# Optimization experiments

Hardware: AMD Instinct MI355X
Metric: run time of the kernel (lower is better)

Reference implementation:

```python
import jax, jax.numpy as jnp
import numpy as np

D_HEAD = 64
KV_HEADS = 8
Q_HEADS = 32
ROPE_BASE = 10000.0


def rope(x):
    # x: (B, S, H, D); pairs are interleaved along last dim, matching torch view(...,D//2,2)
    B, S, H, D = x.shape
    inv_freq = 1.0 / (ROPE_BASE ** (jnp.arange(0, D, 2, dtype=jnp.float32) / D))
    theta = jnp.arange(S, dtype=jnp.float32)[:, None] * inv_freq[None, :]  # (S, D/2)
    cos = jnp.cos(theta)[None, :, None, :]
    sin = jnp.sin(theta)[None, :, None, :]
    xf = x.astype(jnp.float32).reshape(B, S, H, D // 2, 2)
    x1, x2 = xf[..., 0], xf[..., 1]
    out = jnp.stack((x1 * cos - x2 * sin, x1 * sin + x2 * cos), axis=-1)
    return out.reshape(B, S, H, D).astype(x.dtype)


def setup_inputs() -> dict:
    key = jax.random.key(0)
    ks = jax.random.split(key, 5)
    B, S, D = 2, 2048, 2048
    scale = 1.0 / np.sqrt(D)
    return {
        "x": jax.random.normal(ks[0], (B, S, D), dtype=jnp.float32),
        "Wq": jax.random.normal(ks[1], (Q_HEADS * D_HEAD, D), dtype=jnp.float32) * scale,
        "Wk": jax.random.normal(ks[2], (KV_HEADS * D_HEAD, D), dtype=jnp.float32) * scale,
        "Wv": jax.random.normal(ks[3], (KV_HEADS * D_HEAD, D), dtype=jnp.float32) * scale,
        "Wo": jax.random.normal(ks[4], (D, D), dtype=jnp.float32) * scale,
    }


def reference(x, Wq, Wk, Wv, Wo):
    B, S, D = x.shape
    G = Q_HEADS // KV_HEADS  # query heads per kv head

    Q = (x @ Wq.T).reshape(B, S, Q_HEADS, D_HEAD)
    K = (x @ Wk.T).reshape(B, S, KV_HEADS, D_HEAD)
    V = (x @ Wv.T).reshape(B, S, KV_HEADS, D_HEAD)

    Q = rope(Q)
    K = rope(K)

    # (B, KV, G, S, Dh): group g of kv head h corresponds to q head h*G+g,
    # exactly matching repeat_interleave of K/V along head dim.
    Q = Q.transpose(0, 2, 1, 3).reshape(B, KV_HEADS, G, S, D_HEAD)
    K = K.transpose(0, 2, 1, 3)  # (B, KV, S, Dh)
    V = V.transpose(0, 2, 1, 3)

    scores = jnp.einsum("bkgsd,bktd->bkgst", Q, K) / np.sqrt(D_HEAD).astype(np.float32)
    causal_mask = jnp.tril(jnp.ones((S, S), dtype=bool))
    scores = jnp.where(causal_mask, scores, -jnp.inf)
    probs = jax.nn.softmax(scores, axis=-1)
    attn = jnp.einsum("bkgst,bktd->bkgsd", probs, V)

    attn = attn.reshape(B, Q_HEADS, S, D_HEAD).transpose(0, 2, 1, 3).reshape(B, S, D)
    return attn @ Wo.T
```

## Files before the change

kernel.cpp:

```cpp
#include <hip/hip_runtime.h>
#include <stdint.h>

#define S_LEN   2048
#define D_MODEL 2048
#define DKV     512

typedef __attribute__((ext_vector_type(8))) short short8;
typedef __attribute__((ext_vector_type(4))) float f32x4;

__device__ static inline unsigned short f2bf(float f) {
  unsigned u = __builtin_bit_cast(unsigned, f);
  u += 0x7FFFu + ((u >> 16) & 1u);
  return (unsigned short)(u >> 16);
}
__device__ static inline float bf2f(unsigned short h) {
  return __builtin_bit_cast(float, ((unsigned)h) << 16);
}
__device__ static inline unsigned packtrunc2(float f0, float f1) {
  return __builtin_amdgcn_perm(__builtin_bit_cast(unsigned, f1),
                               __builtin_bit_cast(unsigned, f0), 0x07060302u);
}

__device__ static inline void gload_lds16(const void* g, void* lds) {
  __builtin_amdgcn_global_load_lds((const __attribute__((address_space(1))) void*)g,
                                   (__attribute__((address_space(3))) void*)lds,
                                   16, 0, 0);
}

template <int N>
__device__ __forceinline__ void wait_vm() {
  if constexpr (N == 8)      asm volatile("s_waitcnt vmcnt(8)" ::: "memory");
  else if constexpr (N == 6) asm volatile("s_waitcnt vmcnt(6)" ::: "memory");
  else if constexpr (N == 4) asm volatile("s_waitcnt vmcnt(4)" ::: "memory");
  else if constexpr (N == 3) asm volatile("s_waitcnt vmcnt(3)" ::: "memory");
  else                       asm volatile("s_waitcnt vmcnt(0)" ::: "memory");
}

__global__ __launch_bounds__(256) void cvt_all_kernel(
    const float* __restrict__ x, const float* __restrict__ wq, const float* __restrict__ wk,
    const float* __restrict__ wv, const float* __restrict__ wo,
    unsigned short* __restrict__ xb, unsigned short* __restrict__ wqb,
    unsigned short* __restrict__ wkb, unsigned short* __restrict__ wvb,
    unsigned short* __restrict__ wob) {
  int i = blockIdx.x * 256 + threadIdx.x;
  const float* s; unsigned short* d;
  if (i < 1048576)      { s = x;  d = xb;  }
  else if (i < 1572864) { s = wq; d = wqb; i -= 1048576; }
  else if (i < 1703936) { s = wk; d = wkb; i -= 1572864; }
  else if (i < 1835008) { s = wv; d = wvb; i -= 1703936; }
  else                  { s = wo; d = wob; i -= 1835008; }
  const float4 a = ((const float4*)s)[i * 2];
  const float4 b = ((const float4*)s)[i * 2 + 1];
  unsigned short u[8] = {f2bf(a.x), f2bf(a.y), f2bf(a.z), f2bf(a.w),
                         f2bf(b.x), f2bf(b.y), f2bf(b.z), f2bf(b.w)};
  *(uint4*)(d + (size_t)i * 8) = *(const uint4*)u;
}

template <int BM, int CMODE, typename CT>
__device__ __forceinline__ void gemm_deep_body(
    const unsigned short* __restrict__ A, int lda,
    const unsigned short* __restrict__ B, int ldb,
    CT* __restrict__ C, int ldc, int m0, int n0, unsigned short* ldsu) {
  constexpr int MI = BM / 32;
  constexpr int NI = 4;
  constexpr int A_BYTES = BM * 64;
  constexpr int B_BYTES = 256 * 64;
  constexpr int TILE_BYTES = A_BYTES + B_BYTES;
  constexpr int AL = BM / 128;
  constexpr int LOADS = AL + 2;
  constexpr int VMS = 2 * LOADS;

  const int tid  = threadIdx.x;
  const int lane = tid & 63;
  const int w    = tid >> 6;
  const int wm   = w >> 2;
  const int wn   = w & 3;
  const int lcol = lane & 15;
  const int lq   = lane >> 4;
  char* const ldsb = (char*)ldsu;

  const int sl   = (lane & 7) ^ (lane >> 3);
  const int colg = (sl & 3) * 8;
  const unsigned short* gA[AL];
  const unsigned short* gB[2];
#pragma unroll
  for (int L = 0; L < AL; ++L) {
    const int r = 2 * (L * 64 + w * 8 + (lane >> 3)) + (sl >> 2);
    gA[L] = A + (size_t)(m0 + r) * lda + colg;
  }
#pragma unroll
  for (int L = 0; L < 2; ++L) {
    const int r = 2 * (L * 64 + w * 8 + (lane >> 3)) + (sl >> 2);
    gB[L] = B + (size_t)(n0 + r) * ldb + colg;
  }

  auto stage = [&](int tt) {
    char* const sb = ldsb + (tt & 3) * TILE_BYTES;
#pragma unroll
    for (int L = 0; L < AL; ++L)
      gload_lds16(gA[L] + tt * 32, sb + L * 8192 + w * 1024);
#pragma unroll
    for (int L = 0; L < 2; ++L)
      gload_lds16(gB[L] + tt * 32, sb + A_BYTES + L * 8192 + w * 1024);
  };

  const int sR    = (((lcol & 1) << 2) | lq) ^ ((lcol >> 1) & 7);
  const int rdoff = (lcol >> 1) * 128 + sR * 16;

  f32x4 acc[MI][NI] = {};

  auto compute_tile = [&](char* buf) {
    short8 af[MI], bfr[NI];
#pragma unroll
    for (int mi = 0; mi < MI; ++mi)
      af[mi] = *(const short8*)(buf + wm * (MI * 1024) + mi * 1024 + rdoff);
#pragma unroll
    for (int ni = 0; ni < NI; ++ni)
      bfr[ni] = *(const short8*)(buf + A_BYTES + wn * 4096 + ni * 1024 + rdoff);
    __builtin_amdgcn_s_setprio(1);
#pragma unroll
    for (int mi = 0; mi < MI; ++mi)
#pragma unroll
      for (int ni = 0; ni < NI; ++ni)
        acc[mi][ni] = __builtin_amdgcn_mfma_f32_16x16x32_bf16(af[mi], bfr[ni], acc[mi][ni], 0, 0, 0);
    __builtin_amdgcn_s_setprio(0);
  };

  stage(0); stage(1); stage(2);

#define GPHASE(T, VMW, DOSTG)                          \
  do {                                                 \
    wait_vm<VMW>();                                    \
    __builtin_amdgcn_s_barrier();                      \
    asm volatile("" ::: "memory");                     \
    __builtin_amdgcn_sched_barrier(0);                 \
    if (DOSTG) stage((T) + 3);                         \
    compute_tile(ldsb + ((T) & 3) * TILE_BYTES);       \
  } while (0)

  for (int t4 = 0; t4 < 15; ++t4) {
    const int t = t4 * 4;
    GPHASE(t + 0, VMS, true);
    GPHASE(t + 1, VMS, true);
    GPHASE(t + 2, VMS, true);
    GPHASE(t + 3, VMS, true);
  }
  GPHASE(60, VMS,   true);
  GPHASE(61, VMS,   false);
  GPHASE(62, LOADS, false);
  GPHASE(63, 0,     false);
#undef GPHASE

#pragma unroll
  for (int mi = 0; mi < MI; ++mi)
#pragma unroll
    for (int ni = 0; ni < NI; ++ni)
#pragma unroll
      for (int r = 0; r < 4; ++r) {
        const int row = m0 + wm * (MI * 16) + mi * 16 + lq * 4 + r;
        const int col = n0 + wn * 64 + ni * 16 + lcol;
        if constexpr (CMODE == 1) {
          C[((size_t)((row >> 11) * 512 + col)) * 2048 + (row & 2047)] = f2bf(acc[mi][ni][r]);
        } else if constexpr (CMODE == 2) {
          C[(size_t)row * ldc + col] = acc[mi][ni][r];
        } else {
          C[(size_t)row * ldc + col] = f2bf(acc[mi][ni][r]);
        }
      }
}

__global__ __launch_bounds__(512, 2) void qkv_gemm_kernel(
    const unsigned short* __restrict__ x,
    const unsigned short* __restrict__ Wq, const unsigned short* __restrict__ Wk,
    const unsigned short* __restrict__ Wv,
    unsigned short* __restrict__ Qo, unsigned short* __restrict__ Ko,
    unsigned short* __restrict__ Vt) {
  extern __shared__ __align__(16) unsigned short lds[];
  const int bid = blockIdx.x;
  const int swz = (bid & 7) * 24 + (bid >> 3);
  const int mt = swz / 12, nt = swz % 12;
  const int m0 = mt * 256;
  if (nt < 8)
    gemm_deep_body<256, 0, unsigned short>(x, D_MODEL, Wq, D_MODEL, Qo, D_MODEL, m0, nt * 256, lds);
  else if (nt < 10)
    gemm_deep_body<256, 0, unsigned short>(x, D_MODEL, Wk, D_MODEL, Ko, DKV, m0, (nt - 8) * 256, lds);
  else
    gemm_deep_body<256, 1, unsigned short>(x, D_MODEL, Wv, D_MODEL, Vt, DKV, m0, (nt - 10) * 256, lds);
}

__global__ __launch_bounds__(512, 2) void oproj_gemm_kernel(
    const unsigned short* __restrict__ A, const unsigned short* __restrict__ Wo,
    float* __restrict__ C) {
  extern __shared__ __align__(16) unsigned short lds[];
  const int bid = blockIdx.x;
  const int swz = (bid & 7) * 32 + (bid >> 3);
  const int mt = swz >> 3, nt = swz & 7;
  gemm_deep_body<128, 2, float>(A, D_MODEL, Wo, D_MODEL, C, D_MODEL, mt * 128, nt * 256, lds);
}

__global__ __launch_bounds__(256) void rope_both_kernel(unsigned short* __restrict__ Qb,
                                                        unsigned short* __restrict__ Kb) {
  int idx = blockIdx.x * 256 + threadIdx.x;
  unsigned short* X; int lgHalf; float scale;
  if (idx < 4194304) { X = Qb; lgHalf = 10; scale = 0.1803368801111244f; }
  else               { X = Kb; lgHalf = 8;  scale = 1.0f; idx -= 4194304; }
  const int half = 1 << lgHalf;
  const int r  = idx >> lgHalf;
  const int cp = idx & (half - 1);
  const int i  = cp & 31;
  const int s  = r & (S_LEN - 1);
  const float inv = exp2f(-13.287712379549449f * (float)(2 * i) * (1.0f / 64.0f));
  const float th  = (float)s * inv;
  const float c = cosf(th), sn = sinf(th);
  unsigned short* p = X + ((size_t)r << (lgHalf + 1)) + 2 * cp;
  const float x0 = bf2f(p[0]), x1 = bf2f(p[1]);
  p[0] = f2bf((x0 * c - x1 * sn) * scale);
  p[1] = f2bf((x0 * sn + x1 * c) * scale);
}

__global__ __launch_bounds__(256, 2) void attn_kernel(const unsigned short* __restrict__ Q,
                                                      const unsigned short* __restrict__ K,
                                                      const unsigned short* __restrict__ Vt,
                                                      unsigned short* __restrict__ O) {
  const int hq = blockIdx.y;
  const int bb = blockIdx.z;
  const int hk = hq >> 2;
  const int tid  = threadIdx.x;
  const int lane = tid & 63;
  const int w    = tid >> 6;
  const int lcol = lane & 15;
  const int lq   = lane >> 4;
  const int trow = tid >> 2;
  const int tq   = (tid & 3) * 16;

  const int X = blockIdx.x;
  const int qt[4] = {X, 15 - X, 16 + X, 31 - X};

  __shared__ unsigned short Ks[64 * 72];
  __shared__ unsigned short Vts[64 * 72];
  __shared__ unsigned short Ps[4][64 * 72];

  const int prow = w * 16 + lcol;

  uint4 kp0, kp1, vp0, vp1;
  {
    const unsigned short* gk = K + ((size_t)(bb * S_LEN + trow)) * DKV + hk * 64 + tq;
    kp0 = *(const uint4*)gk; kp1 = *(const uint4*)(gk + 8);
    const unsigned short* gv = Vt + ((size_t)(bb * DKV + hk * 64 + trow)) * S_LEN + tq;
    vp0 = *(const uint4*)gv; vp1 = *(const uint4*)(gv + 8);
  }

#pragma unroll
  for (int j = 0; j < 4; ++j) {
    const unsigned short* g = Q + ((size_t)(bb * S_LEN + qt[j] * 64 + trow)) * D_MODEL + hq * 64 + tq;
    *(uint4*)&Ps[j][trow * 72 + tq]     = *(const uint4*)g;
    *(uint4*)&Ps[j][trow * 72 + tq + 8] = *(const uint4*)(g + 8);
  }
  asm volatile("s_waitcnt lgkmcnt(0)" ::: "memory");

  short8 qf[4][2];
#pragma unroll
  for (int j = 0; j < 4; ++j)
#pragma unroll
    for (int ks = 0; ks < 2; ++ks)
      qf[j][ks] = *(const short8*)&Ps[j][prow * 72 + ks * 32 + lq * 8];

  f32x4 Oacc[4][4] = {};
  float lacc[4] = {0.f, 0.f, 0.f, 0.f};

  const int tmax = qt[3];
  for (int t = 0; t <= tmax; ++t) {
    __syncthreads();
    *(uint4*)&Ks[trow * 72 + tq]      = kp0;
    *(uint4*)&Ks[trow * 72 + tq + 8]  = kp1;
    *(uint4*)&Vts[trow * 72 + tq]     = vp0;
    *(uint4*)&Vts[trow * 72 + tq + 8] = vp1;
    if (t < tmax) {
      const int t1 = (t + 1) * 64;
      const unsigned short* gk = K + ((size_t)(bb * S_LEN + t1 + trow)) * DKV + hk * 64 + tq;
      kp0 = *(const uint4*)gk; kp1 = *(const uint4*)(gk + 8);
      const unsigned short* gv = Vt + ((size_t)(bb * DKV + hk * 64 + trow)) * S_LEN + t1 + tq;
      vp0 = *(const uint4*)gv; vp1 = *(const uint4*)(gv + 8);
    }
    __syncthreads();

    bool act[4];
#pragma unroll
    for (int j = 0; j < 4; ++j) act[j] = (t <= qt[j]);

    f32x4 S[4][4] = {};
#pragma unroll
    for (int ks = 0; ks < 2; ++ks)
#pragma unroll
      for (int nt = 0; nt < 4; ++nt) {
        const short8 kf = *(const short8*)&Ks[(nt * 16 + lcol) * 72 + ks * 32 + lq * 8];
#pragma unroll
        for (int j = 0; j < 4; ++j)
          if (act[j])
            S[j][nt] = __builtin_amdgcn_mfma_f32_16x16x32_bf16(kf, qf[j][ks], S[j][nt], 0, 0, 0);
      }

#pragma unroll
    for (int j = 0; j < 4; ++j) {
      if (!act[j]) continue;
      if (t == qt[j]) {
        const int qrow = qt[j] * 64 + prow;
#pragma unroll
        for (int nt = 0; nt < 4; ++nt)
#pragma unroll
          for (int r = 0; r < 4; ++r) {
            const int key = t * 64 + nt * 16 + lq * 4 + r;
            if (key > qrow) S[j][nt][r] = -1e30f;
          }
      }
#pragma unroll
      for (int nt = 0; nt < 4; ++nt) {
        const float p0 = __builtin_amdgcn_exp2f(S[j][nt][0]);
        const float p1 = __builtin_amdgcn_exp2f(S[j][nt][1]);
        const float p2 = __builtin_amdgcn_exp2f(S[j][nt][2]);
        const float p3 = __builtin_amdgcn_exp2f(S[j][nt][3]);
        lacc[j] += (p0 + p1) + (p2 + p3);
        unsigned u2[2] = {packtrunc2(p0, p1), packtrunc2(p2, p3)};
        *(uint2*)&Ps[j][prow * 72 + nt * 16 + lq * 4] = *(const uint2*)u2;
      }
    }
    asm volatile("s_waitcnt lgkmcnt(0)" ::: "memory");

#pragma unroll
    for (int ks = 0; ks < 2; ++ks) {
      short8 pf[4];
#pragma unroll
      for (int j = 0; j < 4; ++j)
        if (act[j]) pf[j] = *(const short8*)&Ps[j][prow * 72 + ks * 32 + lq * 8];
#pragma unroll
      for (int dt = 0; dt < 4; ++dt) {
        const short8 vf = *(const short8*)&Vts[(dt * 16 + lcol) * 72 + ks * 32 + lq * 8];
#pragma unroll
        for (int j = 0; j < 4; ++j)
          if (act[j])
            Oacc[j][dt] = __builtin_amdgcn_mfma_f32_16x16x32_bf16(vf, pf[j], Oacc[j][dt], 0, 0, 0);
      }
    }
  }

#pragma unroll
  for (int j = 0; j < 4; ++j) {
    float l = lacc[j];
    l += __shfl_xor(l, 16);
    l += __shfl_xor(l, 32);
    const float inv = 1.0f / l;
    const int qrow = qt[j] * 64 + prow;
#pragma unroll
    for (int dt = 0; dt < 4; ++dt) {
      unsigned short u[4] = {f2bf(Oacc[j][dt][0] * inv), f2bf(Oacc[j][dt][1] * inv),
                             f2bf(Oacc[j][dt][2] * inv), f2bf(Oacc[j][dt][3] * inv)};
      *(uint2*)&O[(size_t)(bb * S_LEN + qrow) * D_MODEL + hq * 64 + dt * 16 + lq * 4] =
          *(const uint2*)u;
    }
  }
}

extern "C" void kernel_launch(void* const* d_in, const int* in_sizes, int n_in,
                              void* d_out, int out_size, void* d_ws, size_t ws_size,
                              hipStream_t stream) {
  const float* x  = (const float*)d_in[0];
  const float* Wq = (const float*)d_in[1];
  const float* Wk = (const float*)d_in[2];
  const float* Wv = (const float*)d_in[3];
  const float* Wo = (const float*)d_in[4];
  float* out = (float*)d_out;

  unsigned short* Qb  = (unsigned short*)d_ws;
  unsigned short* Kb  = Qb  + (size_t)4096 * 2048;
  unsigned short* Vtg = Kb  + (size_t)4096 * 512;
  unsigned short* Ab  = Vtg + (size_t)1024 * 2048;
  unsigned short* xb  = Ab  + (size_t)4096 * 2048;
  unsigned short* Wqb = xb  + (size_t)4096 * 2048;
  unsigned short* Wkb = Wqb + (size_t)2048 * 2048;
  unsigned short* Wvb = Wkb + (size_t)512 * 2048;
  unsigned short* Wob = Wvb + (size_t)512 * 2048;

  static bool attr_set = false;
  if (!attr_set) {
    hipFuncSetAttribute(reinterpret_cast<const void*>(qkv_gemm_kernel),
                        hipFuncAttributeMaxDynamicSharedMemorySize, 131072);
    hipFuncSetAttribute(reinterpret_cast<const void*>(oproj_gemm_kernel),
                        hipFuncAttributeMaxDynamicSharedMemorySize, 98304);
    attr_set = true;
  }

  cvt_all_kernel<<<9216, 256, 0, stream>>>(x, Wq, Wk, Wv, Wo, xb, Wqb, Wkb, Wvb, Wob);

  qkv_gemm_kernel<<<192, 512, 131072, stream>>>(xb, Wqb, Wkb, Wvb, Qb, Kb, Vtg);
  rope_both_kernel<<<20480, 256, 0, stream>>>(Qb, Kb);
  attn_kernel<<<dim3(8, 32, 2), 256, 0, stream>>>(Qb, Kb, Vtg, Ab);
  oproj_gemm_kernel<<<256, 512, 98304, stream>>>(Ab, Wob, out);
}
```

Before: 286.1 us.

## Restructure attention: two q-tiles per block, register P via permlane, double-buffered K/V

The attention kernel now handles two query tiles per block instead of four, and the grid doubles to keep full coverage. Softmax probabilities are repacked into MFMA operand layout in registers using v_permlane32/16 swaps, which removes the P round-trip through LDS. Q fragments are loaded straight from global memory, K/V LDS tiles are double-buffered so one barrier per iteration replaces two, and launch bounds are raised to allow four blocks per CU. The aim is lower LDS traffic, fewer syncs and higher occupancy, at the cost of reloading K/V twice as often per q-head.

```diff
diff --git a/kernel.cpp b/kernel.cpp
--- a/kernel.cpp
+++ b/kernel.cpp
@@ -7,6 +7,7 @@
 
 typedef __attribute__((ext_vector_type(8))) short short8;
 typedef __attribute__((ext_vector_type(4))) float f32x4;
+typedef __attribute__((ext_vector_type(4))) unsigned uint4v;
 
 __device__ static inline unsigned short f2bf(float f) {
   unsigned u = __builtin_bit_cast(unsigned, f);
@@ -34,6 +35,13 @@
   else if constexpr (N == 4) asm volatile("s_waitcnt vmcnt(4)" ::: "memory");
   else if constexpr (N == 3) asm volatile("s_waitcnt vmcnt(3)" ::: "memory");
   else                       asm volatile("s_waitcnt vmcnt(0)" ::: "memory");
+}
+
+__device__ static inline void pl32swap(unsigned& a, unsigned& b) {
+  asm volatile("v_permlane32_swap_b32 %0, %1" : "+v"(a), "+v"(b));
+}
+__device__ static inline void pl16swap(unsigned& a, unsigned& b) {
+  asm volatile("v_permlane16_swap_b32 %0, %1" : "+v"(a), "+v"(b));
 }
 
 __global__ __launch_bounds__(256) void cvt_all_kernel(
@@ -218,7 +226,7 @@
   p[1] = f2bf((x0 * sn + x1 * c) * scale);
 }
 
-__global__ __launch_bounds__(256, 2) void attn_kernel(const unsigned short* __restrict__ Q,
+__global__ __launch_bounds__(256, 4) void attn_kernel(const unsigned short* __restrict__ Q,
                                                       const unsigned short* __restrict__ K,
                                                       const unsigned short* __restrict__ Vt,
                                                       unsigned short* __restrict__ O) {
@@ -233,14 +241,24 @@
   const int trow = tid >> 2;
   const int tq   = (tid & 3) * 16;
 
-  const int X = blockIdx.x;
-  const int qt[4] = {X, 15 - X, 16 + X, 31 - X};
-
-  __shared__ unsigned short Ks[64 * 72];
-  __shared__ unsigned short Vts[64 * 72];
-  __shared__ unsigned short Ps[4][64 * 72];
+  const int X   = blockIdx.x;
+  const int qt0 = X, qt1 = 31 - X;
+
+  __shared__ unsigned short Ks[2][64 * 72];
+  __shared__ unsigned short Vts[2][64 * 72];
 
   const int prow = w * 16 + lcol;
+
+  short8 qf[2][2];
+  {
+    const unsigned short* g0 = Q + ((size_t)(bb * S_LEN + qt0 * 64 + prow)) * D_MODEL + hq * 64;
+    const unsigned short* g1 = Q + ((size_t)(bb * S_LEN + qt1 * 64 + prow)) * D_MODEL + hq * 64;
+#pragma unroll
+    for (int ks = 0; ks < 2; ++ks) {
+      qf[0][ks] = *(const short8*)(g0 + ks * 32 + lq * 8);
+      qf[1][ks] = *(const short8*)(g1 + ks * 32 + lq * 8);
+    }
+  }
 
   uint4 kp0, kp1, vp0, vp1;
   {
@@ -250,31 +268,38 @@
     vp0 = *(const uint4*)gv; vp1 = *(const uint4*)(gv + 8);
   }
 
-#pragma unroll
-  for (int j = 0; j < 4; ++j) {
-    const unsigned short* g = Q + ((size_t)(bb * S_LEN + qt[j] * 64 + trow)) * D_MODEL + hq * 64 + tq;
-    *(uint4*)&Ps[j][trow * 72 + tq]     = *(const uint4*)g;
-    *(uint4*)&Ps[j][trow * 72 + tq + 8] = *(const uint4*)(g + 8);
-  }
-  asm volatile("s_waitcnt lgkmcnt(0)" ::: "memory");
-
-  short8 qf[4][2];
-#pragma unroll
-  for (int j = 0; j < 4; ++j)
-#pragma unroll
-    for (int ks = 0; ks < 2; ++ks)
-      qf[j][ks] = *(const short8*)&Ps[j][prow * 72 + ks * 32 + lq * 8];
-
-  f32x4 Oacc[4][4] = {};
-  float lacc[4] = {0.f, 0.f, 0.f, 0.f};
-
-  const int tmax = qt[3];
+  f32x4 Oacc[2][4] = {};
+  float lacc[2] = {0.f, 0.f};
+
+  auto softmax_frag = [&](f32x4* Sv, float& lac, short8* pfo) {
+    unsigned dd[4][2];
+#pragma unroll
+    for (int nt = 0; nt < 4; ++nt) {
+      const float p0 = __builtin_amdgcn_exp2f(Sv[nt][0]);
+      const float p1 = __builtin_amdgcn_exp2f(Sv[nt][1]);
+      const float p2 = __builtin_amdgcn_exp2f(Sv[nt][2]);
+      const float p3 = __builtin_amdgcn_exp2f(Sv[nt][3]);
+      lac += (p0 + p1) + (p2 + p3);
+      dd[nt][0] = packtrunc2(p0, p1);
+      dd[nt][1] = packtrunc2(p2, p3);
+    }
+    pl32swap(dd[0][0], dd[1][0]); pl32swap(dd[0][1], dd[1][1]);
+    pl32swap(dd[2][0], dd[3][0]); pl32swap(dd[2][1], dd[3][1]);
+    pl16swap(dd[0][0], dd[1][0]); pl16swap(dd[0][1], dd[1][1]);
+    pl16swap(dd[2][0], dd[3][0]); pl16swap(dd[2][1], dd[3][1]);
+    const uint4v va = {dd[0][0], dd[0][1], dd[1][0], dd[1][1]};
+    const uint4v vb = {dd[2][0], dd[2][1], dd[3][0], dd[3][1]};
+    pfo[0] = __builtin_bit_cast(short8, va);
+    pfo[1] = __builtin_bit_cast(short8, vb);
+  };
+
+  const int tmax = qt1;
   for (int t = 0; t <= tmax; ++t) {
-    __syncthreads();
-    *(uint4*)&Ks[trow * 72 + tq]      = kp0;
-    *(uint4*)&Ks[trow * 72 + tq + 8]  = kp1;
-    *(uint4*)&Vts[trow * 72 + tq]     = vp0;
-    *(uint4*)&Vts[trow * 72 + tq + 8] = vp1;
+    const int bs = t & 1;
+    *(uint4*)&Ks[bs][trow * 72 + tq]      = kp0;
+    *(uint4*)&Ks[bs][trow * 72 + tq + 8]  = kp1;
+    *(uint4*)&Vts[bs][trow * 72 + tq]     = vp0;
+    *(uint4*)&Vts[bs][trow * 72 + tq + 8] = vp1;
     if (t < tmax) {
       const int t1 = (t + 1) * 64;
       const unsigned short* gk = K + ((size_t)(bb * S_LEN + t1 + trow)) * DKV + hk * 64 + tq;
@@ -282,74 +307,59 @@
       const unsigned short* gv = Vt + ((size_t)(bb * DKV + hk * 64 + trow)) * S_LEN + t1 + tq;
       vp0 = *(const uint4*)gv; vp1 = *(const uint4*)(gv + 8);
     }
-    __syncthreads();
-
-    bool act[4];
-#pragma unroll
-    for (int j = 0; j < 4; ++j) act[j] = (t <= qt[j]);
-
-    f32x4 S[4][4] = {};
+    asm volatile("s_waitcnt lgkmcnt(0)" ::: "memory");
+    __builtin_amdgcn_s_barrier();
+    __builtin_amdgcn_sched_barrier(0);
+
+    const bool a0 = (t <= qt0);
+
+    f32x4 S0[4] = {}, S1[4] = {};
 #pragma unroll
     for (int ks = 0; ks < 2; ++ks)
 #pragma unroll
       for (int nt = 0; nt < 4; ++nt) {
-        const short8 kf = *(const short8*)&Ks[(nt * 16 + lcol) * 72 + ks * 32 + lq * 8];
-#pragma unroll
-        for (int j = 0; j < 4; ++j)
-          if (act[j])
-            S[j][nt] = __builtin_amdgcn_mfma_f32_16x16x32_bf16(kf, qf[j][ks], S[j][nt], 0, 0, 0);
+        const short8 kf = *(const short8*)&Ks[bs][(nt * 16 + lcol) * 72 + ks * 32 + lq * 8];
+        if (a0) S0[nt] = __builtin_amdgcn_mfma_f32_16x16x32_bf16(kf, qf[0][ks], S0[nt], 0, 0, 0);
+        S1[nt] = __builtin_amdgcn_mfma_f32_16x16x32_bf16(kf, qf[1][ks], S1[nt], 0, 0, 0);
       }
 
-#pragma unroll
-    for (int j = 0; j < 4; ++j) {
-      if (!act[j]) continue;
-      if (t == qt[j]) {
-        const int qrow = qt[j] * 64 + prow;
-#pragma unroll
-        for (int nt = 0; nt < 4; ++nt)
-#pragma unroll
-          for (int r = 0; r < 4; ++r) {
-            const int key = t * 64 + nt * 16 + lq * 4 + r;
-            if (key > qrow) S[j][nt][r] = -1e30f;
-          }
+    if (t == qt0) {
+#pragma unroll
+      for (int nt = 0; nt < 4; ++nt)
+#pragma unroll
+        for (int r = 0; r < 4; ++r)
+          if (nt * 16 + lq * 4 + r > prow) S0[nt][r] = -1e30f;
+    }
+    if (t == qt1) {
+#pragma unroll
+      for (int nt = 0; nt < 4; ++nt)
+#pragma unroll
+        for (int r = 0; r < 4; ++r)
+          if (nt * 16 + lq * 4 + r > prow) S1[nt][r] = -1e30f;
+    }
+
+    short8 pf0[2], pf1[2];
+    if (a0) softmax_frag(S0, lacc[0], pf0);
+    softmax_frag(S1, lacc[1], pf1);
+
+#pragma unroll
+    for (int ks = 0; ks < 2; ++ks)
+#pragma unroll
+      for (int dt = 0; dt < 4; ++dt) {
+        const short8 vf = *(const short8*)&Vts[bs][(dt * 16 + lcol) * 72 + ks * 32 + lq * 8];
+        if (a0) Oacc[0][dt] = __builtin_amdgcn_mfma_f32_16x16x32_bf16(vf, pf0[ks], Oacc[0][dt], 0, 0, 0);
+        Oacc[1][dt] = __builtin_amdgcn_mfma_f32_16x16x32_bf16(vf, pf1[ks], Oacc[1][dt], 0, 0, 0);
       }
-#pragma unroll
-      for (int nt = 0; nt < 4; ++nt) {
-        const float p0 = __builtin_amdgcn_exp2f(S[j][nt][0]);
-        const float p1 = __builtin_amdgcn_exp2f(S[j][nt][1]);
-        const float p2 = __builtin_amdgcn_exp2f(S[j][nt][2]);
-        const float p3 = __builtin_amdgcn_exp2f(S[j][nt][3]);
-        lacc[j] += (p0 + p1) + (p2 + p3);
-        unsigned u2[2] = {packtrunc2(p0, p1), packtrunc2(p2, p3)};
-        *(uint2*)&Ps[j][prow * 72 + nt * 16 + lq * 4] = *(const uint2*)u2;
-      }
-    }
-    asm volatile("s_waitcnt lgkmcnt(0)" ::: "memory");
-
-#pragma unroll
-    for (int ks = 0; ks < 2; ++ks) {
-      short8 pf[4];
-#pragma unroll
-      for (int j = 0; j < 4; ++j)
-        if (act[j]) pf[j] = *(const short8*)&Ps[j][prow * 72 + ks * 32 + lq * 8];
-#pragma unroll
-      for (int dt = 0; dt < 4; ++dt) {
-        const short8 vf = *(const short8*)&Vts[(dt * 16 + lcol) * 72 + ks * 32 + lq * 8];
-#pragma unroll
-        for (int j = 0; j < 4; ++j)
-          if (act[j])
-            Oacc[j][dt] = __builtin_amdgcn_mfma_f32_16x16x32_bf16(vf, pf[j], Oacc[j][dt], 0, 0, 0);
-      }
-    }
-  }
-
-#pragma unroll
-  for (int j = 0; j < 4; ++j) {
+  }
+
+  const int qts[2] = {qt0, qt1};
+#pragma unroll
+  for (int j = 0; j < 2; ++j) {
     float l = lacc[j];
     l += __shfl_xor(l, 16);
     l += __shfl_xor(l, 32);
     const float inv = 1.0f / l;
-    const int qrow = qt[j] * 64 + prow;
+    const int qrow = qts[j] * 64 + prow;
 #pragma unroll
     for (int dt = 0; dt < 4; ++dt) {
       unsigned short u[4] = {f2bf(Oacc[j][dt][0] * inv), f2bf(Oacc[j][dt][1] * inv),
@@ -393,6 +403,6 @@
 
   qkv_gemm_kernel<<<192, 512, 131072, stream>>>(xb, Wqb, Wkb, Wvb, Qb, Kb, Vtg);
   rope_both_kernel<<<20480, 256, 0, stream>>>(Qb, Kb);
-  attn_kernel<<<dim3(8, 32, 2), 256, 0, stream>>>(Qb, Kb, Vtg, Ab);
+  attn_kernel<<<dim3(16, 32, 2), 256, 0, stream>>>(Qb, Kb, Vtg, Ab);
   oproj_gemm_kernel<<<256, 512, 98304, stream>>>(Ab, Wob, out);
 }
```

Measured after the change: 482.4 us. 68.6% more time.
